# Kernel tuning notes

Measured on AMD Instinct MI355X. Metric: run time of the kernel, lower is better.

The kernel has to match this reference:

```python
import jax, jax.numpy as jnp
import numpy as np

MODES = 16

def setup_inputs() -> dict:
    key = jax.random.key(0)
    k1, k2 = jax.random.split(key)
    x = jax.random.normal(k1, (16, 32, 256, 256), dtype=jnp.float32)
    weights = jax.random.normal(k2, (32, 32, MODES, MODES, 2), dtype=jnp.float32) * 0.1
    return {"x": x, "weights": weights}

def reference(x, weights):
    # x: [B, Ci, H, W]; weights: [Ci, Co, m, m, 2]
    B, Ci, H, W = x.shape
    m = weights.shape[2]
    Co = weights.shape[1]
    x_ft = jnp.fft.rfft2(x, axes=(-2, -1))  # [B, Ci, H, W//2+1] complex
    w_c = jax.lax.complex(weights[..., 0], weights[..., 1])  # [Ci, Co, m, m]
    low = jnp.einsum('bixy,ioxy->boxy', x_ft[:, :, :m, :m], w_c)  # [B, Co, m, m]
    out_ft = jnp.zeros((B, Co, H, W // 2 + 1), dtype=x_ft.dtype)
    out_ft = out_ft.at[:, :, :m, :m].set(low)
    return jnp.fft.irfft2(out_ft, s=(H, W), axes=(-2, -1)).astype(x.dtype)
```

## Files before the change

kernel.cpp:

```cpp
#include <hip/hip_runtime.h>

typedef float v4 __attribute__((ext_vector_type(4)));

#define TWO_PI_256 0.024543692606170259f


__global__ __launch_bounds__(256) void k0_trig(float* __restrict__ Tg) {
  const int k = threadIdx.x;
#pragma unroll
  for (int kx = 0; kx < 16; ++kx) {
    float sv, cv;
    sincosf((float)((kx * k) & 255) * TWO_PI_256, &sv, &cv);
    Tg[k * 32 + 2 * kx] = cv;
    Tg[k * 32 + 2 * kx + 1] = -sv;
  }
}

typedef __attribute__((address_space(1))) const unsigned int gas_u32;
typedef __attribute__((address_space(3))) unsigned int las_u32;

__global__ __launch_bounds__(256, 4) void k1_dftw(const float* __restrict__ x,
                                                  const float* __restrict__ Tg,
                                                  float* __restrict__ F) {
  __shared__ float Ts[32][32];
  __shared__ float Xs[32][132];
  const int tid = threadIdx.x;
  const int cg = tid & 7;
  const int rg = tid >> 3;
  const int o0 = cg * 4;
  const int r0 = rg * 4;
  const long rblk = (long)blockIdx.x * 128;
  float acc[4][4] = {};
  for (int kc = 0; kc < 256; kc += 32) {
    __syncthreads();
    __builtin_amdgcn_global_load_lds(
        (gas_u32*)(Tg + kc * 32 + tid * 4),
        (las_u32*)((unsigned int*)&Ts[0][0] + (tid >> 6) * 256), 16, 0, 0);
#pragma unroll
    for (int p = 0; p < 4; ++p) {
      const int row = (tid >> 3) + p * 32;
      const int k4 = (tid & 7) * 4;
      const v4 v = *(const v4*)&x[(rblk + row) * 256 + kc + k4];
      Xs[k4 + 0][row] = v[0];
      Xs[k4 + 1][row] = v[1];
      Xs[k4 + 2][row] = v[2];
      Xs[k4 + 3][row] = v[3];
    }
    __syncthreads();
#pragma unroll
    for (int k = 0; k < 32; k += 4) {
      v4 xv[4], tv[4];
#pragma unroll
      for (int i = 0; i < 4; ++i) xv[i] = *(const v4*)&Xs[k + i][r0];
#pragma unroll
      for (int i = 0; i < 4; ++i) tv[i] = *(const v4*)&Ts[k + i][o0];
#pragma unroll
      for (int i = 0; i < 4; ++i)
#pragma unroll
        for (int r = 0; r < 4; ++r)
#pragma unroll
          for (int c = 0; c < 4; ++c) acc[r][c] += xv[i][r] * tv[i][c];
    }
  }
#pragma unroll
  for (int r = 0; r < 4; ++r) {
    v4 o;
#pragma unroll
    for (int c = 0; c < 4; ++c) o[c] = acc[r][c];
    *(v4*)&F[(rblk + r0 + r) * 32 + o0] = o;
  }
}

__global__ __launch_bounds__(256) void k2_dfth(const float* __restrict__ F,
                                               float* __restrict__ X) {
  __shared__ float2 tbl[256];
  __shared__ float Fs[64][36];
  const int tid = threadIdx.x;
  const int bc = blockIdx.x;
  {
    float sv, cv;
    sincosf((float)tid * TWO_PI_256, &sv, &cv);
    tbl[tid] = make_float2(cv, sv);
  }
  const int kx = tid & 15;
  const int ky = tid >> 4;
  float xr = 0.f, xi = 0.f;
  const float* Fb = F + (long)bc * 8192;
  for (int hc = 0; hc < 256; hc += 64) {
    __syncthreads();
#pragma unroll
    for (int p = 0; p < 2; ++p) {
      const int h = (tid >> 3) + p * 32;
      const int j = (tid & 7) * 4;
      *(v4*)&Fs[h][j] = *(const v4*)&Fb[(hc + h) * 32 + j];
    }
    __syncthreads();
#pragma unroll 8
    for (int hl = 0; hl < 64; ++hl) {
      const int h = hc + hl;
      const float2 f = *(const float2*)&Fs[hl][2 * kx];
      const float2 w = tbl[(ky * h) & 255];
      xr += f.x * w.x + f.y * w.y;
      xi += f.y * w.x - f.x * w.y;
    }
  }
  *(float2*)&X[((long)bc * 256 + tid) * 2] = make_float2(xr, xi);
}

__global__ __launch_bounds__(256) void k3_mix(const float* __restrict__ X,
                                              const float* __restrict__ Wt,
                                              float* __restrict__ Y) {
  const int t = threadIdx.x;
  const int co = blockIdx.x;
  const int b = blockIdx.y;
  float yr = 0.f, yi = 0.f;
#pragma unroll 4
  for (int ci = 0; ci < 32; ++ci) {
    const float2 xv = *(const float2*)&X[((long)(b * 32 + ci) * 256 + t) * 2];
    const float2 wv = *(const float2*)&Wt[((long)(ci * 32 + co) * 256 + t) * 2];
    yr += xv.x * wv.x - xv.y * wv.y;
    yi += xv.x * wv.y + xv.y * wv.x;
  }
  *(float2*)&Y[((long)(b * 32 + co) * 256 + t) * 2] = make_float2(yr, yi);
}

__global__ __launch_bounds__(256) void k4_inv(const float* __restrict__ Y,
                                              float* __restrict__ out) {
  __shared__ float2 tbl[256];
  __shared__ float2 Ys[256];
  __shared__ float G[256][36];
  const int tid = threadIdx.x;
  const int co = blockIdx.x;
  const int b = blockIdx.y;
  {
    float sv, cv;
    sincosf((float)tid * TWO_PI_256, &sv, &cv);
    tbl[tid] = make_float2(cv, sv);
  }
  Ys[tid] = *(const float2*)&Y[((long)(b * 32 + co) * 256 + tid) * 2];
  __syncthreads();
  {
    float gr[16] = {}, gi[16] = {};
#pragma unroll 4
    for (int ky = 0; ky < 16; ++ky) {
      const float2 w = tbl[(ky * tid) & 255];
#pragma unroll
      for (int kx = 0; kx < 16; ++kx) {
        const float2 yv = Ys[ky * 16 + kx];
        gr[kx] += yv.x * w.x - yv.y * w.y;
        gi[kx] += yv.x * w.y + yv.y * w.x;
      }
    }
#pragma unroll
    for (int kx = 0; kx < 16; ++kx)
      *(float2*)&G[tid][2 * kx] = make_float2(gr[kx], gi[kx]);
  }
  __syncthreads();
  const int s = tid & 127;
  const int hh = tid >> 7;
  float cs[16], sn[16];
#pragma unroll
  for (int kx = 1; kx < 16; ++kx) {
    const float2 w = tbl[(kx * s) & 255];
    cs[kx] = 2.f * w.x;
    sn[kx] = 2.f * w.y;
  }
  const float inv = 1.f / 65536.f;
  float* __restrict__ ob = out + (long)(b * 32 + co) * 65536;
  for (int h = hh; h < 256; h += 2) {
    float gr[16], gi[16];
#pragma unroll
    for (int j = 0; j < 8; ++j) {
      const v4 q = *(const v4*)&G[h][4 * j];
      gr[2 * j] = q[0];
      gi[2 * j] = q[1];
      gr[2 * j + 1] = q[2];
      gi[2 * j + 1] = q[3];
    }
    float a = gr[0];
    float bs = 0.f;
#pragma unroll
    for (int kx = 1; kx < 16; ++kx) {
      a += gr[kx] * cs[kx];
      bs += gi[kx] * sn[kx];
    }
    if (s == 0) {
      float a128 = gr[0];
#pragma unroll
      for (int kx = 1; kx < 16; ++kx)
        a128 += (kx & 1) ? -2.f * gr[kx] : 2.f * gr[kx];
      ob[h * 256] = a * inv;
      ob[h * 256 + 128] = a128 * inv;
    } else {
      ob[h * 256 + s] = (a - bs) * inv;
      ob[h * 256 + 256 - s] = (a + bs) * inv;
    }
  }
}

extern "C" void kernel_launch(void* const* d_in, const int* in_sizes, int n_in,
                              void* d_out, int out_size, void* d_ws, size_t ws_size,
                              hipStream_t stream) {
  const float* x = (const float*)d_in[0];
  const float* wt = (const float*)d_in[1];
  float* out = (float*)d_out;
  float* F = (float*)d_ws;
  float* X = F + 4194304;
  float* Yv = X + 262144;
  float* Tg = Yv + 262144;
  k0_trig<<<1, 256, 0, stream>>>(Tg);
  k1_dftw<<<1024, 256, 0, stream>>>(x, Tg, F);
  k2_dfth<<<512, 256, 0, stream>>>(F, X);
  k3_mix<<<dim3(32, 16), 256, 0, stream>>>(X, wt, Yv);
  k4_inv<<<dim3(32, 16), 256, 0, stream>>>(Yv, out);
}
```

Baseline: 297.3 us.

## Move width DFT onto bf16 MFMA with split hi/lo precision

```diff
diff --git a/kernel.cpp b/kernel.cpp
--- a/kernel.cpp
+++ b/kernel.cpp
@@ -1,74 +1,113 @@
 #include <hip/hip_runtime.h>
 
 typedef float v4 __attribute__((ext_vector_type(4)));
+typedef float f32x4 __attribute__((ext_vector_type(4)));
+typedef short bf16x8 __attribute__((ext_vector_type(8)));
 
 #define TWO_PI_256 0.024543692606170259f
 
 
-__global__ __launch_bounds__(256) void k0_trig(float* __restrict__ Tg) {
+__device__ __forceinline__ unsigned short f2bf(float f) {
+  const unsigned int u = __float_as_uint(f);
+  return (unsigned short)((u + 0x7fffu + ((u >> 16) & 1u)) >> 16);
+}
+__device__ __forceinline__ float bf2f(unsigned short h) {
+  return __uint_as_float(((unsigned int)h) << 16);
+}
+
+__global__ __launch_bounds__(256) void k0_trig(unsigned short* __restrict__ Th,
+                                               unsigned short* __restrict__ Tl) {
   const int k = threadIdx.x;
 #pragma unroll
   for (int kx = 0; kx < 16; ++kx) {
     float sv, cv;
     sincosf((float)((kx * k) & 255) * TWO_PI_256, &sv, &cv);
-    Tg[k * 32 + 2 * kx] = cv;
-    Tg[k * 32 + 2 * kx + 1] = -sv;
+    const float vals[2] = {cv, -sv};
+#pragma unroll
+    for (int p = 0; p < 2; ++p) {
+      const int o = 2 * kx + p;
+      const unsigned short hi = f2bf(vals[p]);
+      Th[o * 256 + k] = hi;
+      Tl[o * 256 + k] = f2bf(vals[p] - bf2f(hi));
+    }
   }
 }
 
 typedef __attribute__((address_space(1))) const unsigned int gas_u32;
 typedef __attribute__((address_space(3))) unsigned int las_u32;
 
-__global__ __launch_bounds__(256, 4) void k1_dftw(const float* __restrict__ x,
-                                                  const float* __restrict__ Tg,
-                                                  float* __restrict__ F) {
-  __shared__ float Ts[32][32];
-  __shared__ float Xs[32][132];
+__global__ __launch_bounds__(256) void k1_dftw(const float* __restrict__ x,
+                                               const unsigned short* __restrict__ Th,
+                                               const unsigned short* __restrict__ Tl,
+                                               float* __restrict__ F) {
+  __shared__ float Xs[128 * 32];
+  __shared__ __align__(16) unsigned short Ts[2][32 * 264];
   const int tid = threadIdx.x;
-  const int cg = tid & 7;
-  const int rg = tid >> 3;
-  const int o0 = cg * 4;
-  const int r0 = rg * 4;
+  const int lane = tid & 63;
+  const int w = tid >> 6;
   const long rblk = (long)blockIdx.x * 128;
-  float acc[4][4] = {};
+  {
+    const int o = tid >> 3, kb = (tid & 7) * 32;
+#pragma unroll
+    for (int f = 0; f < 2; ++f) {
+      const unsigned short* src = (f ? Tl : Th) + o * 256 + kb;
+      unsigned short* dst = &Ts[f][o * 264 + kb];
+#pragma unroll
+      for (int j = 0; j < 32; j += 8)
+        *(bf16x8*)(dst + j) = *(const bf16x8*)(src + j);
+    }
+  }
+  const int q = lane >> 4;
+  const int n16 = lane & 15;
+  f32x4 acc[2][2] = {};
   for (int kc = 0; kc < 256; kc += 32) {
     __syncthreads();
-    __builtin_amdgcn_global_load_lds(
-        (gas_u32*)(Tg + kc * 32 + tid * 4),
-        (las_u32*)((unsigned int*)&Ts[0][0] + (tid >> 6) * 256), 16, 0, 0);
-#pragma unroll
-    for (int p = 0; p < 4; ++p) {
-      const int row = (tid >> 3) + p * 32;
-      const int k4 = (tid & 7) * 4;
-      const v4 v = *(const v4*)&x[(rblk + row) * 256 + kc + k4];
-      Xs[k4 + 0][row] = v[0];
-      Xs[k4 + 1][row] = v[1];
-      Xs[k4 + 2][row] = v[2];
-      Xs[k4 + 3][row] = v[3];
-    }
-    __syncthreads();
-#pragma unroll
-    for (int k = 0; k < 32; k += 4) {
-      v4 xv[4], tv[4];
-#pragma unroll
-      for (int i = 0; i < 4; ++i) xv[i] = *(const v4*)&Xs[k + i][r0];
-#pragma unroll
-      for (int i = 0; i < 4; ++i) tv[i] = *(const v4*)&Ts[k + i][o0];
-#pragma unroll
-      for (int i = 0; i < 4; ++i)
-#pragma unroll
-        for (int r = 0; r < 4; ++r)
-#pragma unroll
-          for (int c = 0; c < 4; ++c) acc[r][c] += xv[i][r] * tv[i][c];
-    }
-  }
-#pragma unroll
-  for (int r = 0; r < 4; ++r) {
-    v4 o;
-#pragma unroll
-    for (int c = 0; c < 4; ++c) o[c] = acc[r][c];
-    *(v4*)&F[(rblk + r0 + r) * 32 + o0] = o;
-  }
+#pragma unroll
+    for (int i = 0; i < 4; ++i) {
+      const int r0 = w * 32 + i * 8;
+      __builtin_amdgcn_global_load_lds(
+          (gas_u32*)(x + (rblk + r0 + (lane >> 3)) * 256 + kc + (lane & 7) * 4),
+          (las_u32*)((unsigned int*)Xs + r0 * 32), 16, 0, 0);
+    }
+    __syncthreads();
+    bf16x8 bh[2], bl[2];
+#pragma unroll
+    for (int nt = 0; nt < 2; ++nt) {
+      const int o = nt * 16 + n16;
+      bh[nt] = *(const bf16x8*)&Ts[0][o * 264 + kc + q * 8];
+      bl[nt] = *(const bf16x8*)&Ts[1][o * 264 + kc + q * 8];
+    }
+#pragma unroll
+    for (int mt = 0; mt < 2; ++mt) {
+      const int m = w * 32 + mt * 16 + n16;
+      const float* ap = &Xs[m * 32 + q * 8];
+      const v4 a0 = *(const v4*)ap;
+      const v4 a1 = *(const v4*)(ap + 4);
+      const float af[8] = {a0[0], a0[1], a0[2], a0[3], a1[0], a1[1], a1[2], a1[3]};
+      bf16x8 ah, al;
+#pragma unroll
+      for (int j = 0; j < 8; ++j) {
+        const unsigned short h = f2bf(af[j]);
+        ah[j] = (short)h;
+        al[j] = (short)f2bf(af[j] - bf2f(h));
+      }
+#pragma unroll
+      for (int nt = 0; nt < 2; ++nt) {
+        acc[mt][nt] = __builtin_amdgcn_mfma_f32_16x16x32_bf16(ah, bh[nt], acc[mt][nt], 0, 0, 0);
+        acc[mt][nt] = __builtin_amdgcn_mfma_f32_16x16x32_bf16(al, bh[nt], acc[mt][nt], 0, 0, 0);
+        acc[mt][nt] = __builtin_amdgcn_mfma_f32_16x16x32_bf16(ah, bl[nt], acc[mt][nt], 0, 0, 0);
+      }
+    }
+  }
+#pragma unroll
+  for (int mt = 0; mt < 2; ++mt)
+#pragma unroll
+    for (int nt = 0; nt < 2; ++nt)
+#pragma unroll
+      for (int r = 0; r < 4; ++r) {
+        const long row = rblk + w * 32 + mt * 16 + q * 4 + r;
+        F[row * 32 + nt * 16 + n16] = acc[mt][nt][r];
+      }
 }
 
 __global__ __launch_bounds__(256) void k2_dfth(const float* __restrict__ F,
@@ -171,11 +210,11 @@
     float gr[16], gi[16];
 #pragma unroll
     for (int j = 0; j < 8; ++j) {
-      const v4 q = *(const v4*)&G[h][4 * j];
-      gr[2 * j] = q[0];
-      gi[2 * j] = q[1];
-      gr[2 * j + 1] = q[2];
-      gi[2 * j + 1] = q[3];
+      const v4 qv = *(const v4*)&G[h][4 * j];
+      gr[2 * j] = qv[0];
+      gi[2 * j] = qv[1];
+      gr[2 * j + 1] = qv[2];
+      gi[2 * j + 1] = qv[3];
     }
     float a = gr[0];
     float bs = 0.f;
@@ -207,9 +246,10 @@
   float* F = (float*)d_ws;
   float* X = F + 4194304;
   float* Yv = X + 262144;
-  float* Tg = Yv + 262144;
-  k0_trig<<<1, 256, 0, stream>>>(Tg);
-  k1_dftw<<<1024, 256, 0, stream>>>(x, Tg, F);
+  unsigned short* Th = (unsigned short*)(Yv + 262144);
+  unsigned short* Tl = Th + 8192;
+  k0_trig<<<1, 256, 0, stream>>>(Th, Tl);
+  k1_dftw<<<1024, 256, 0, stream>>>(x, Th, Tl, F);
   k2_dfth<<<512, 256, 0, stream>>>(F, X);
   k3_mix<<<dim3(32, 16), 256, 0, stream>>>(X, wt, Yv);
   k4_inv<<<dim3(32, 16), 256, 0, stream>>>(Yv, out);
```

Measured after the change: 296.0 us. About the same (-0.4%).
